# Performance work log

Hardware: AMD Instinct MI355X
Metric: run time of the kernel (lower is better)

Reference implementation:

```python
import jax, jax.numpy as jnp
import numpy as np

_EPS = 1e-5

def _ln(x, scale, shift):
    # Faithful to the module's custom layer norm: variance term is the SUM of
    # squared deviations over the feature dim (not the mean), and the affine is
    # scale * normed + shift with scale=b*, shift=s* (argument order as in source).
    m = jnp.mean(x, axis=-1, keepdims=True)
    d = x - m
    ssq = jnp.sum(d * d, axis=-1, keepdims=True)
    return scale * (d / jnp.sqrt(ssq + _EPS)) + shift


def setup_inputs() -> dict:
    key = jax.random.key(0)
    ks = jax.random.split(key, 12)
    B, T, I, H = 64, 512, 512, 512
    f32 = jnp.float32
    return {
        "x": jax.random.normal(ks[0], (B, T, I), f32),
        "hx": jax.random.normal(ks[1], (B, H), f32),
        "cx": jax.random.normal(ks[2], (B, H), f32),
        "Wi": jax.random.normal(ks[3], (4 * H, I), f32) / np.float32(np.sqrt(I)),
        "Wh": jax.random.normal(ks[4], (4 * H, H), f32) / np.float32(np.sqrt(H)),
        "bias": jax.random.normal(ks[5], (4 * H,), f32) * 0.1,
        "b1": jax.random.normal(ks[6], (4 * H,), f32) * 0.1,
        "b2": jax.random.normal(ks[7], (4 * H,), f32) * 0.1,
        "b3": jax.random.normal(ks[8], (H,), f32) * 0.1,
        "s1": 1.0 + jax.random.normal(ks[9], (4 * H,), f32) * 0.1,
        "s2": 1.0 + jax.random.normal(ks[10], (4 * H,), f32) * 0.1,
        "s3": 1.0 + jax.random.normal(ks[11], (H,), f32) * 0.1,
    }


def reference(x, hx, cx, Wi, Wh, bias, b1, b2, b3, s1, s2, s3):
    # x: [B, T, I] (batch_first). Work in time-major for the scan.
    xT = jnp.swapaxes(x, 0, 1)  # [T, B, I]
    # The input-projection layer norm has no cross-time dependency -> precompute.
    gi = _ln(jnp.einsum('tbi,gi->tbg', xT, Wi), b1, s1)  # [T, B, 4H]

    def step(carry, gi_t):
        h, c = carry
        gates = gi_t + _ln(h @ Wh.T, b2, s2) + bias  # [B, 4H]
        i, f, g, o = jnp.split(gates, 4, axis=-1)
        i = jax.nn.sigmoid(i)
        f = jax.nn.sigmoid(f)
        g = jnp.tanh(g)
        o = jax.nn.sigmoid(o)
        c_new = _ln(f * c + i * g, b3, s3)
        h_new = o * jnp.tanh(c_new)
        return (h_new, c_new), h_new

    (hy, cy), ys = jax.lax.scan(step, (hx, cx), gi)
    output = jnp.swapaxes(ys, 0, 1)  # back to [B, T, H]
    return output, hy, cy
```

## Files before the change

### kernel.cpp

```cpp
#include <hip/hip_runtime.h>
#include <cstdint>
#include <cstddef>


typedef float  f32x4 __attribute__((ext_vector_type(4)));
typedef __bf16 bf16x8 __attribute__((ext_vector_type(8)));
typedef unsigned int u32x4 __attribute__((ext_vector_type(4)));
typedef unsigned short u16x4 __attribute__((ext_vector_type(4)));

#define DEV __device__ __forceinline__

#define LD4_AGENT(dst, p) asm volatile("global_load_dwordx4 %0, %1, off sc1" : "=v"(dst) : "v"(p) : "memory")
#define ISSUE_U64(dst, p) asm volatile("global_load_dwordx2 %0, %1, off sc1" : "=v"(dst) : "v"(p) : "memory")
#define WAIT_VM(N) do{ asm volatile("s_waitcnt vmcnt(" #N ")" ::: "memory"); \
                       __builtin_amdgcn_sched_barrier(0);}while(0)
#define VM0_FENCE() do{ asm volatile("s_waitcnt vmcnt(0)" ::: "memory"); \
                        __builtin_amdgcn_sched_barrier(0); }while(0)

DEV unsigned short f2b(float f){
  unsigned int u = __builtin_bit_cast(unsigned int, f);
  unsigned int r = (u + 0x7FFFu + ((u >> 16) & 1u)) >> 16;
  return (unsigned short)r;
}
DEV float b2f(unsigned short s){
  unsigned int u = ((unsigned int)s) << 16;
  return __builtin_bit_cast(float, u);
}
DEV float tanh_fast(float x){
  const float e = __expf(2.f * x);
  return 1.f - 2.f * __builtin_amdgcn_rcpf(e + 1.f);
}
DEV float sigmoid_fast(float x){
  return __builtin_amdgcn_rcpf(1.f + __expf(-x));
}

__global__ __launch_bounds__(256) void conv_bf16(const float* __restrict__ src,
                                                 unsigned short* __restrict__ dst,
                                                 int n4){
  int i = blockIdx.x * 256 + threadIdx.x;
  if (i >= n4) return;
  f32x4 v = ((const f32x4*)src)[i];
  u16x4 o;
  #pragma unroll
  for (int j = 0; j < 4; ++j) o[j] = f2b(v[j]);
  ((u16x4*)dst)[i] = o;
}

__global__ __launch_bounds__(256, 2) void gemm_gi(const unsigned short* __restrict__ Xb,
                                                  const unsigned short* __restrict__ Wib,
                                                  unsigned short* __restrict__ Gp){
  __shared__ unsigned short As[128 * 48];
  __shared__ unsigned short Bs[128 * 48];
  const int tid = threadIdx.x;
  const int m0 = blockIdx.x * 128;
  const int n0 = blockIdx.y * 128;
  const int w = tid >> 6, lane = tid & 63;
  const int lr = lane & 15, lq = lane >> 4;
  const int wm = (w & 1) * 64, wn = (w >> 1) * 64;
  const int sr = tid >> 2;
  const int sc = (tid & 3) * 8;
  const unsigned short* gx = Xb + (size_t)(m0 + sr) * 512 + sc;
  const unsigned short* gw = Wib + (size_t)(n0 + sr) * 512 + sc;
  f32x4 acc[4][4] = {};
  for (int kb = 0; kb < 16; ++kb){
    u32x4 a0 = *(const u32x4*)(gx + kb * 32);
    u32x4 a1 = *(const u32x4*)(gx + 64 * 512 + kb * 32);
    u32x4 b0 = *(const u32x4*)(gw + kb * 32);
    u32x4 b1 = *(const u32x4*)(gw + 64 * 512 + kb * 32);
    __syncthreads();
    *(u32x4*)&As[sr * 48 + sc] = a0;
    *(u32x4*)&As[(sr + 64) * 48 + sc] = a1;
    *(u32x4*)&Bs[sr * 48 + sc] = b0;
    *(u32x4*)&Bs[(sr + 64) * 48 + sc] = b1;
    __syncthreads();
    bf16x8 af[4], bfv[4];
    #pragma unroll
    for (int mi = 0; mi < 4; ++mi) af[mi] = *(const bf16x8*)&As[(wm + mi * 16 + lr) * 48 + lq * 8];
    #pragma unroll
    for (int ni = 0; ni < 4; ++ni) bfv[ni] = *(const bf16x8*)&Bs[(wn + ni * 16 + lr) * 48 + lq * 8];
    #pragma unroll
    for (int mi = 0; mi < 4; ++mi)
      #pragma unroll
      for (int ni = 0; ni < 4; ++ni)
        acc[mi][ni] = __builtin_amdgcn_mfma_f32_16x16x32_bf16(af[mi], bfv[ni], acc[mi][ni], 0, 0, 0);
  }
  #pragma unroll
  for (int mi = 0; mi < 4; ++mi){
    const int rowb = m0 + wm + mi * 16 + lq * 4;
    #pragma unroll
    for (int ni = 0; ni < 4; ++ni){
      const int col = n0 + wn + ni * 16 + lr;
      #pragma unroll
      for (int r = 0; r < 4; ++r)
        Gp[(size_t)(rowb + r) * 2048 + col] = f2b(acc[mi][ni][r]);
    }
  }
}

__global__ __launch_bounds__(256) void ln_rows(unsigned short* __restrict__ G,
                                               const float* __restrict__ b1,
                                               const float* __restrict__ s1){
  const int row = blockIdx.x;
  const int tid = threadIdx.x;
  unsigned short* rp = G + (size_t)row * 2048 + tid * 8;
  u32x4 raw = *(const u32x4*)rp;
  float x[8];
  #pragma unroll
  for (int j = 0; j < 8; ++j){
    unsigned int word = raw[j >> 1];
    unsigned short us = (j & 1) ? (unsigned short)(word >> 16) : (unsigned short)(word & 0xFFFF);
    x[j] = b2f(us);
  }
  float s = 0.f, q = 0.f;
  #pragma unroll
  for (int j = 0; j < 8; ++j){ s += x[j]; q += x[j] * x[j]; }
  #pragma unroll
  for (int o = 1; o < 64; o <<= 1){ s += __shfl_xor(s, o); q += __shfl_xor(q, o); }
  __shared__ float ps[4][2];
  const int wv = tid >> 6;
  if ((tid & 63) == 0){ ps[wv][0] = s; ps[wv][1] = q; }
  __syncthreads();
  s = ps[0][0] + ps[1][0] + ps[2][0] + ps[3][0];
  q = ps[0][1] + ps[1][1] + ps[2][1] + ps[3][1];
  const float mu = s * (1.f / 2048.f);
  const float inv = rsqrtf((q - s * mu) + 1e-5f);
  const float* b1p = b1 + tid * 8;
  const float* s1p = s1 + tid * 8;
  u32x4 outw;
  #pragma unroll
  for (int j = 0; j < 4; ++j){
    float y0 = b1p[2 * j]     * ((x[2 * j]     - mu) * inv) + s1p[2 * j];
    float y1 = b1p[2 * j + 1] * ((x[2 * j + 1] - mu) * inv) + s1p[2 * j + 1];
    outw[j] = (unsigned int)f2b(y0) | ((unsigned int)f2b(y1) << 16);
  }
  *(u32x4*)rp = outw;
}

__global__ __launch_bounds__(512, 2) void lstm_rec(
    const unsigned short* __restrict__ Gi,
    const unsigned short* __restrict__ Whb,
    const float* __restrict__ bias,
    const float* __restrict__ b2, const float* __restrict__ s2,
    const float* __restrict__ b3, const float* __restrict__ s3,
    const float* __restrict__ hx,
    const float* __restrict__ cx,
    unsigned int* __restrict__ hbuf,
    unsigned long long* __restrict__ pF,
    unsigned long long* __restrict__ pA,
    unsigned long long* __restrict__ pCs,
    float* __restrict__ out){
  const int tid = threadIdx.x;
  const int tm = (blockIdx.x >> 1) & 3;
  const int ks = ((blockIdx.x >> 3) << 1) | (blockIdx.x & 1);
  const int w = tid >> 6;
  const int lane = tid & 63;
  const int lr = lane & 15, lq = lane >> 4;

  const int type = w >> 1;
  const int jloc = (w & 1) * 16 + lr;
  const int row_g = type * 512 + ks * 32 + jloc;
  const float b2r = b2[row_g];
  const float sbr = s2[row_g] + bias[row_g];

  bf16x8 bfr[16];
  {
    const unsigned short* wr = Whb + (size_t)row_g * 512 + lq * 8;
    #pragma unroll
    for (int kk = 0; kk < 16; ++kk) bfr[kk] = *(const bf16x8*)(wr + kk * 32);
  }

  const int cs = tid >> 5;
  const int cj = tid & 31;
  const int hcol = ks * 32 + cj;
  const int bidx = tm * 16 + cs;
  float c_val = cx[(size_t)bidx * 512 + hcol];
  const float b3j = b3[hcol], s3j = s3[hcol];

  const int psmp = 2 * w + (lane >> 5);
  const int pidx = lane & 31;
  const int pl_slice = (lane >> 1) & 15;
  const int pl_kind  = lane & 1;

  float b3c[16], s3c[16];
  #pragma unroll
  for (int q = 0; q < 4; ++q)
    #pragma unroll
    for (int j = 0; j < 4; ++j){
      const int c = 4 * pidx + 128 * q + j;
      b3c[4 * q + j] = b3[c];
      s3c[4 * q + j] = s3[c];
    }

  __shared__ unsigned short hlds[16 * 520];
  __shared__ float act[4][32][17];
  __shared__ float redA[8][16][2];
  __shared__ float stAl[16][2];

  float cc_own = 0.f, o_own = 0.f;

  for (int t = 0; t < 512; ++t){
    float giv[4];
    #pragma unroll
    for (int r = 0; r < 4; ++r){
      const int b = tm * 16 + lq * 4 + r;
      giv[r] = b2f(Gi[((size_t)b * 512 + t) * 2048 + row_g]);
    }

    if (t == 0){
      const float* hr = hx + (size_t)(tm * 16 + psmp) * 512;
      #pragma unroll
      for (int q = 0; q < 4; ++q){
        f32x4 hv4 = *(const f32x4*)(hr + 4 * pidx + 128 * q);
        unsigned long long pk = 0;
        #pragma unroll
        for (int j = 0; j < 4; ++j)
          pk |= (unsigned long long)f2b(hv4[j]) << (16 * j);
        *(unsigned long long*)&hlds[psmp * 520 + 4 * pidx + 128 * q] = pk;
      }
    } else {
      const unsigned int tg = (unsigned)t;
      const unsigned long long* fp = pF + (size_t)(t & 1) * 64 + tm * 16 + (lane & 15);
      const unsigned long long* sp =
          pCs + ((size_t)(t & 1) * 4 + tm) * 512 + pl_slice * 32 + psmp * 2 + pl_kind;
      unsigned long long fa, sa, fb, sb;
      unsigned long long sv;
      ISSUE_U64(fa, fp); ISSUE_U64(sa, sp);
      __builtin_amdgcn_s_sleep(12);
      ISSUE_U64(fb, fp); ISSUE_U64(sb, sp);
      for (;;){
        WAIT_VM(2);
        bool ok = ((unsigned)fa == tg) & ((unsigned)(sa >> 32) == tg);
        if (__all((int)ok)){ sv = sa; break; }
        ISSUE_U64(fa, fp); ISSUE_U64(sa, sp);
        WAIT_VM(2);
        ok = ((unsigned)fb == tg) & ((unsigned)(sb >> 32) == tg);
        if (__all((int)ok)){ sv = sb; break; }
        ISSUE_U64(fb, fp); ISSUE_U64(sb, sp);
      }
      const unsigned int* hsrc =
          hbuf + (size_t)(t & 1) * 32768 + (size_t)(tm * 16 + psmp) * 512;
      u32x4 pay[4];
      #pragma unroll
      for (int q = 0; q < 4; ++q) LD4_AGENT(pay[q], hsrc + 4 * pidx + 128 * q);
      float pv = __builtin_bit_cast(float, (unsigned)sv);
      #pragma unroll
      for (int o = 2; o < 32; o <<= 1) pv += __shfl_xor(pv, o);
      const float ov = __shfl_xor(pv, 1);
      const float S = pl_kind ? ov : pv;
      const float Q = pl_kind ? pv : ov;
      const float mu = S * (1.f / 512.f);
      const float inv = rsqrtf((Q - S * mu) + 1e-5f);
      c_val = b3j * ((cc_own - mu) * inv) + s3j;
      const float h_self = o_own * tanh_fast(c_val);
      out[((size_t)bidx * 512 + (t - 1)) * 512 + hcol] = h_self;
      VM0_FENCE();
      asm volatile("" :: "v"(fa), "v"(sa), "v"(fb), "v"(sb));
      #pragma unroll
      for (int q = 0; q < 4; ++q){
        unsigned long long pk = 0;
        #pragma unroll
        for (int j = 0; j < 4; ++j){
          const unsigned int v = pay[q][j];
          const float ccv = b2f((unsigned short)(v & 0xFFFF));
          const float oov = b2f((unsigned short)(v >> 16));
          const float h = oov * tanh_fast(b3c[4 * q + j] * ((ccv - mu) * inv) + s3c[4 * q + j]);
          pk |= (unsigned long long)f2b(h) << (16 * j);
        }
        *(unsigned long long*)&hlds[psmp * 520 + 4 * pidx + 128 * q] = pk;
      }
    }
    __syncthreads();

    f32x4 acc = {0.f, 0.f, 0.f, 0.f};
    #pragma unroll
    for (int kk = 0; kk < 16; ++kk){
      bf16x8 af = *(const bf16x8*)&hlds[lr * 520 + lq * 8 + kk * 32];
      acc = __builtin_amdgcn_mfma_f32_16x16x32_bf16(af, bfr[kk], acc, 0, 0, 0);
    }
    #pragma unroll
    for (int r = 0; r < 4; ++r){
      float s = acc[r], q = acc[r] * acc[r];
      #pragma unroll
      for (int o = 1; o < 16; o <<= 1){ s += __shfl_xor(s, o); q += __shfl_xor(q, o); }
      if (lr == 0){ redA[w][lq * 4 + r][0] = s; redA[w][lq * 4 + r][1] = q; }
    }
    __syncthreads();

    unsigned long long* slotA = pA + ((size_t)(t & 1) * 4 + tm) * 512;
    const unsigned int atag = (unsigned)(t + 1);
    if (w == 0 && lane < 32){
      const int smp = lane >> 1, kd = lane & 1;
      float Sp = 0.f;
      #pragma unroll
      for (int w2 = 0; w2 < 8; ++w2) Sp += redA[w2][smp][kd];
      const unsigned long long pvs = ((unsigned long long)atag << 32) |
          (unsigned long long)__builtin_bit_cast(unsigned int, Sp);
      __hip_atomic_store(slotA + (size_t)ks * 32 + lane, pvs,
                         __ATOMIC_RELAXED, __HIP_MEMORY_SCOPE_AGENT);
    }
    unsigned long long aa, ab;
    {
      const unsigned long long* ap = slotA + pl_slice * 32 + psmp * 2 + pl_kind;
      unsigned long long av;
      ISSUE_U64(aa, ap);
      __builtin_amdgcn_s_sleep(12);
      ISSUE_U64(ab, ap);
      for (;;){
        WAIT_VM(1);
        if (__all((int)((unsigned)(aa >> 32) == atag))){ av = aa; break; }
        ISSUE_U64(aa, ap);
        WAIT_VM(1);
        if (__all((int)((unsigned)(ab >> 32) == atag))){ av = ab; break; }
        ISSUE_U64(ab, ap);
      }
      float pv = __builtin_bit_cast(float, (unsigned)av);
      #pragma unroll
      for (int o = 2; o < 32; o <<= 1) pv += __shfl_xor(pv, o);
      const float ov = __shfl_xor(pv, 1);
      const float S = pl_kind ? ov : pv;
      const float Q = pl_kind ? pv : ov;
      if ((lane & 31) == 0){
        const float mu = S * (1.f / 2048.f);
        stAl[psmp][0] = mu;
        stAl[psmp][1] = rsqrtf((Q - S * mu) + 1e-5f);
      }
    }
    __syncthreads();

    #pragma unroll
    for (int r = 0; r < 4; ++r){
      const int s0 = lq * 4 + r;
      const float nv = (acc[r] - stAl[s0][0]) * stAl[s0][1];
      const float gv = giv[r] + b2r * nv + sbr;
      float a;
      if (type == 2) a = tanh_fast(gv);
      else           a = sigmoid_fast(gv);
      act[type][jloc][s0] = a;
    }
    __syncthreads();

    const float i_g = act[0][cj][cs];
    const float f_g = act[1][cj][cs];
    const float g_g = act[2][cj][cs];
    const float o_g = act[3][cj][cs];
    const float cc = f_g * c_val + i_g * g_g;
    const unsigned int ntag = (unsigned)(t + 1);
    const size_t np = (size_t)((t + 1) & 1);
    {
      const unsigned int pv32 = (unsigned int)f2b(cc) | ((unsigned int)f2b(o_g) << 16);
      __hip_atomic_store(hbuf + np * 32768 + (size_t)bidx * 512 + hcol, pv32,
                         __ATOMIC_RELAXED, __HIP_MEMORY_SCOPE_AGENT);
    }
    float sC = cc, qC = cc * cc;
    #pragma unroll
    for (int o = 1; o < 32; o <<= 1){ sC += __shfl_xor(sC, o); qC += __shfl_xor(qC, o); }
    unsigned long long* slotC = pCs + (np * 4 + tm) * 512;
    if ((lane & 31) < 2){
      const float v = (lane & 1) ? qC : sC;
      const unsigned long long pvs = ((unsigned long long)ntag << 32) |
          (unsigned long long)__builtin_bit_cast(unsigned int, v);
      __hip_atomic_store(slotC + (size_t)ks * 32 + cs * 2 + (lane & 1), pvs,
                         __ATOMIC_RELAXED, __HIP_MEMORY_SCOPE_AGENT);
    }
    VM0_FENCE();
    asm volatile("" :: "v"(aa), "v"(ab));
    __syncthreads();
    if (tid == 0)
      __hip_atomic_store(pF + np * 64 + tm * 16 + ks, (unsigned long long)ntag,
                         __ATOMIC_RELAXED, __HIP_MEMORY_SCOPE_AGENT);
    cc_own = cc; o_own = o_g;
  }

  {
    const unsigned long long* sp =
        pCs + ((size_t)0 * 4 + tm) * 512 + pl_slice * 32 + psmp * 2 + pl_kind;
    unsigned long long sv;
    for (;;){
      sv = __hip_atomic_load(sp, __ATOMIC_RELAXED, __HIP_MEMORY_SCOPE_AGENT);
      if (__all((int)((unsigned)(sv >> 32) == 512u))) break;
      __builtin_amdgcn_s_sleep(2);
    }
    float pv = __builtin_bit_cast(float, (unsigned)sv);
    #pragma unroll
    for (int o = 2; o < 32; o <<= 1) pv += __shfl_xor(pv, o);
    const float ov = __shfl_xor(pv, 1);
    const float S = pl_kind ? ov : pv;
    const float Q = pl_kind ? pv : ov;
    const float mu = S * (1.f / 512.f);
    const float inv = rsqrtf((Q - S * mu) + 1e-5f);
    const float cn = b3j * ((cc_own - mu) * inv) + s3j;
    const float h = o_own * tanh_fast(cn);
    out[((size_t)bidx * 512 + 511) * 512 + hcol] = h;
    out[16777216u + (size_t)bidx * 512 + hcol] = h;
    out[16777216u + 32768u + (size_t)bidx * 512 + hcol] = cn;
  }
}

extern "C" void kernel_launch(void* const* d_in, const int* in_sizes, int n_in,
                              void* d_out, int out_size, void* d_ws, size_t ws_size,
                              hipStream_t stream){
  (void)in_sizes; (void)n_in; (void)out_size; (void)ws_size;
  const float* x    = (const float*)d_in[0];
  const float* hx   = (const float*)d_in[1];
  const float* cx   = (const float*)d_in[2];
  const float* Wi   = (const float*)d_in[3];
  const float* Wh   = (const float*)d_in[4];
  const float* bias = (const float*)d_in[5];
  const float* b1   = (const float*)d_in[6];
  const float* b2   = (const float*)d_in[7];
  const float* b3   = (const float*)d_in[8];
  const float* s1   = (const float*)d_in[9];
  const float* s2   = (const float*)d_in[10];
  const float* s3   = (const float*)d_in[11];
  float* out = (float*)d_out;
  char* ws = (char*)d_ws;

  unsigned short*     xb   = (unsigned short*)(ws);
  unsigned short*     wib  = (unsigned short*)(ws + 33554432);
  unsigned short*     whb  = (unsigned short*)(ws + 35651584);
  unsigned short*     gp   = (unsigned short*)(ws + 37748736);
  unsigned int*       hbuf = (unsigned int*)(ws + 171966464);
  unsigned long long* pF   = (unsigned long long*)(ws + 172228608);
  unsigned long long* pA   = (unsigned long long*)(ws + 172490752);
  unsigned long long* pCs  = (unsigned long long*)(ws + 172523520);

  hipMemsetAsync(pF, 0, 327680, stream);
  conv_bf16<<<16384, 256, 0, stream>>>(x,  xb,  4194304);
  conv_bf16<<<1024,  256, 0, stream>>>(Wi, wib, 262144);
  conv_bf16<<<1024,  256, 0, stream>>>(Wh, whb, 262144);
  gemm_gi<<<dim3(256, 16, 1), 256, 0, stream>>>(xb, wib, gp);
  ln_rows<<<32768, 256, 0, stream>>>(gp, b1, s1);
  lstm_rec<<<64, 512, 0, stream>>>(gp, whb, bias, b2, s2, b3, s3, hx, cx,
                                   hbuf, pF, pA, pCs, out);
}
```

Baseline: 3.090 ms.

## Compute recurrent LayerNorm stats locally via Gram matrix, removing cross-block exchange

The sum and sum-of-squares of h@Wh^T across all 2048 gate outputs are rewritten algebraically. The sum becomes h·(column sums of Wh), and the squared sum becomes h^T (Wh^T Wh) h, using a 512x512 Gram matrix and column-sum vector precomputed by new transpose and gram GEMM kernels. Each block can then compute the LayerNorm statistics locally, which drops the per-timestep inter-block atomic publish and spin-wait on pA. In exchange each step does four extra MFMA tiles per wave reading the Gram matrix from global memory. Precision also changes, since the Gram matrix is stored in bf16 and the variance is computed as Q - S*mu.

```diff
diff --git a/kernel.cpp b/kernel.cpp
--- a/kernel.cpp
+++ b/kernel.cpp
@@ -136,9 +136,96 @@
   *(u32x4*)rp = outw;
 }
 
-__global__ __launch_bounds__(512, 2) void lstm_rec(
+__global__ __launch_bounds__(256) void transpose_wh(const unsigned short* __restrict__ src,
+                                                    unsigned short* __restrict__ dst,
+                                                    float* __restrict__ wbar){
+  __shared__ unsigned short t[64][65];
+  const int k0 = blockIdx.x * 64;
+  const int d0 = blockIdx.y * 64;
+  const int tr = threadIdx.x >> 2;
+  const int c  = threadIdx.x & 3;
+  const int tc = c * 16;
+  u32x4 a = *(const u32x4*)(src + (size_t)(k0 + tr) * 512 + d0 + tc);
+  u32x4 b = *(const u32x4*)(src + (size_t)(k0 + tr) * 512 + d0 + tc + 8);
+  #pragma unroll
+  for (int j = 0; j < 4; ++j){
+    t[tr][tc + 2 * j]         = (unsigned short)(a[j] & 0xFFFF);
+    t[tr][tc + 2 * j + 1]     = (unsigned short)(a[j] >> 16);
+    t[tr][tc + 8 + 2 * j]     = (unsigned short)(b[j] & 0xFFFF);
+    t[tr][tc + 8 + 2 * j + 1] = (unsigned short)(b[j] >> 16);
+  }
+  __syncthreads();
+  unsigned short tmp[16];
+  float s = 0.f;
+  #pragma unroll
+  for (int j = 0; j < 16; ++j){ tmp[j] = t[tc + j][tr]; s += b2f(tmp[j]); }
+  s += __shfl_xor(s, 1); s += __shfl_xor(s, 2);
+  if (c == 0) atomicAdd(&wbar[d0 + tr], s);
+  u32x4 o0, o1;
+  #pragma unroll
+  for (int j = 0; j < 4; ++j){
+    o0[j] = (unsigned)tmp[2 * j]     | ((unsigned)tmp[2 * j + 1] << 16);
+    o1[j] = (unsigned)tmp[8 + 2 * j] | ((unsigned)tmp[8 + 2 * j + 1] << 16);
+  }
+  *(u32x4*)(dst + (size_t)(d0 + tr) * 2048 + k0 + tc) = o0;
+  *(u32x4*)(dst + (size_t)(d0 + tr) * 2048 + k0 + tc + 8) = o1;
+}
+
+__global__ __launch_bounds__(256, 2) void gemm_gram(const unsigned short* __restrict__ WhT,
+                                                    unsigned short* __restrict__ Gb){
+  __shared__ unsigned short As[128 * 48];
+  __shared__ unsigned short Bs[128 * 48];
+  const int tid = threadIdx.x;
+  const int m0 = blockIdx.x * 128;
+  const int n0 = blockIdx.y * 128;
+  const int w = tid >> 6, lane = tid & 63;
+  const int lr = lane & 15, lq = lane >> 4;
+  const int wm = (w & 1) * 64, wn = (w >> 1) * 64;
+  const int sr = tid >> 2;
+  const int sc = (tid & 3) * 8;
+  const unsigned short* gx = WhT + (size_t)(m0 + sr) * 2048 + sc;
+  const unsigned short* gw = WhT + (size_t)(n0 + sr) * 2048 + sc;
+  f32x4 acc[4][4] = {};
+  for (int kb = 0; kb < 64; ++kb){
+    u32x4 a0 = *(const u32x4*)(gx + kb * 32);
+    u32x4 a1 = *(const u32x4*)(gx + 64 * 2048 + kb * 32);
+    u32x4 b0 = *(const u32x4*)(gw + kb * 32);
+    u32x4 b1 = *(const u32x4*)(gw + 64 * 2048 + kb * 32);
+    __syncthreads();
+    *(u32x4*)&As[sr * 48 + sc] = a0;
+    *(u32x4*)&As[(sr + 64) * 48 + sc] = a1;
+    *(u32x4*)&Bs[sr * 48 + sc] = b0;
+    *(u32x4*)&Bs[(sr + 64) * 48 + sc] = b1;
+    __syncthreads();
+    bf16x8 af[4], bfv[4];
+    #pragma unroll
+    for (int mi = 0; mi < 4; ++mi) af[mi] = *(const bf16x8*)&As[(wm + mi * 16 + lr) * 48 + lq * 8];
+    #pragma unroll
+    for (int ni = 0; ni < 4; ++ni) bfv[ni] = *(const bf16x8*)&Bs[(wn + ni * 16 + lr) * 48 + lq * 8];
+    #pragma unroll
+    for (int mi = 0; mi < 4; ++mi)
+      #pragma unroll
+      for (int ni = 0; ni < 4; ++ni)
+        acc[mi][ni] = __builtin_amdgcn_mfma_f32_16x16x32_bf16(af[mi], bfv[ni], acc[mi][ni], 0, 0, 0);
+  }
+  #pragma unroll
+  for (int mi = 0; mi < 4; ++mi){
+    const int rowb = m0 + wm + mi * 16 + lq * 4;
+    #pragma unroll
+    for (int ni = 0; ni < 4; ++ni){
+      const int col = n0 + wn + ni * 16 + lr;
+      #pragma unroll
+      for (int r = 0; r < 4; ++r)
+        Gb[(size_t)(rowb + r) * 512 + col] = f2b(acc[mi][ni][r]);
+    }
+  }
+}
+
+__global__ __launch_bounds__(512, 1) void lstm_rec(
     const unsigned short* __restrict__ Gi,
     const unsigned short* __restrict__ Whb,
+    const unsigned short* __restrict__ Gb,
+    const float* __restrict__ wbar,
     const float* __restrict__ bias,
     const float* __restrict__ b2, const float* __restrict__ s2,
     const float* __restrict__ b3, const float* __restrict__ s3,
@@ -146,7 +233,6 @@
     const float* __restrict__ cx,
     unsigned int* __restrict__ hbuf,
     unsigned long long* __restrict__ pF,
-    unsigned long long* __restrict__ pA,
     unsigned long long* __restrict__ pCs,
     float* __restrict__ out){
   const int tid = threadIdx.x;
@@ -168,6 +254,10 @@
     #pragma unroll
     for (int kk = 0; kk < 16; ++kk) bfr[kk] = *(const bf16x8*)(wr + kk * 32);
   }
+  const unsigned short* grow = Gb + (size_t)(w * 64 + lr) * 512 + lq * 8;
+  float wbarc[4];
+  #pragma unroll
+  for (int ni = 0; ni < 4; ++ni) wbarc[ni] = wbar[w * 64 + ni * 16 + lr];
 
   const int cs = tid >> 5;
   const int cj = tid & 31;
@@ -272,57 +362,45 @@
     __syncthreads();
 
     f32x4 acc = {0.f, 0.f, 0.f, 0.f};
+    f32x4 accv[4] = {};
     #pragma unroll
     for (int kk = 0; kk < 16; ++kk){
-      bf16x8 af = *(const bf16x8*)&hlds[lr * 520 + lq * 8 + kk * 32];
-      acc = __builtin_amdgcn_mfma_f32_16x16x32_bf16(af, bfr[kk], acc, 0, 0, 0);
+      bf16x8 hf = *(const bf16x8*)&hlds[lr * 520 + lq * 8 + kk * 32];
+      acc = __builtin_amdgcn_mfma_f32_16x16x32_bf16(hf, bfr[kk], acc, 0, 0, 0);
+      #pragma unroll
+      for (int ni = 0; ni < 4; ++ni){
+        bf16x8 gf = *(const bf16x8*)(grow + (size_t)ni * 16 * 512 + kk * 32);
+        accv[ni] = __builtin_amdgcn_mfma_f32_16x16x32_bf16(hf, gf, accv[ni], 0, 0, 0);
+      }
     }
     #pragma unroll
     for (int r = 0; r < 4; ++r){
-      float s = acc[r], q = acc[r] * acc[r];
-      #pragma unroll
-      for (int o = 1; o < 16; o <<= 1){ s += __shfl_xor(s, o); q += __shfl_xor(q, o); }
-      if (lr == 0){ redA[w][lq * 4 + r][0] = s; redA[w][lq * 4 + r][1] = q; }
-    }
-    __syncthreads();
-
-    unsigned long long* slotA = pA + ((size_t)(t & 1) * 4 + tm) * 512;
-    const unsigned int atag = (unsigned)(t + 1);
+      const int srow = lq * 4 + r;
+      float qp = 0.f, sp = 0.f;
+      #pragma unroll
+      for (int ni = 0; ni < 4; ++ni){
+        const float hval = b2f(hlds[srow * 520 + w * 64 + ni * 16 + lr]);
+        qp += accv[ni][r] * hval;
+        sp += wbarc[ni] * hval;
+      }
+      #pragma unroll
+      for (int o = 1; o < 16; o <<= 1){ qp += __shfl_xor(qp, o); sp += __shfl_xor(sp, o); }
+      if (lr == 0){ redA[w][srow][0] = sp; redA[w][srow][1] = qp; }
+    }
+    __syncthreads();
+
     if (w == 0 && lane < 32){
       const int smp = lane >> 1, kd = lane & 1;
-      float Sp = 0.f;
-      #pragma unroll
-      for (int w2 = 0; w2 < 8; ++w2) Sp += redA[w2][smp][kd];
-      const unsigned long long pvs = ((unsigned long long)atag << 32) |
-          (unsigned long long)__builtin_bit_cast(unsigned int, Sp);
-      __hip_atomic_store(slotA + (size_t)ks * 32 + lane, pvs,
-                         __ATOMIC_RELAXED, __HIP_MEMORY_SCOPE_AGENT);
-    }
-    unsigned long long aa, ab;
-    {
-      const unsigned long long* ap = slotA + pl_slice * 32 + psmp * 2 + pl_kind;
-      unsigned long long av;
-      ISSUE_U64(aa, ap);
-      __builtin_amdgcn_s_sleep(12);
-      ISSUE_U64(ab, ap);
-      for (;;){
-        WAIT_VM(1);
-        if (__all((int)((unsigned)(aa >> 32) == atag))){ av = aa; break; }
-        ISSUE_U64(aa, ap);
-        WAIT_VM(1);
-        if (__all((int)((unsigned)(ab >> 32) == atag))){ av = ab; break; }
-        ISSUE_U64(ab, ap);
-      }
-      float pv = __builtin_bit_cast(float, (unsigned)av);
-      #pragma unroll
-      for (int o = 2; o < 32; o <<= 1) pv += __shfl_xor(pv, o);
-      const float ov = __shfl_xor(pv, 1);
-      const float S = pl_kind ? ov : pv;
-      const float Q = pl_kind ? pv : ov;
-      if ((lane & 31) == 0){
+      float P = 0.f;
+      #pragma unroll
+      for (int w2 = 0; w2 < 8; ++w2) P += redA[w2][smp][kd];
+      const float ov = __shfl_xor(P, 1);
+      const float S = kd ? ov : P;
+      const float Q = kd ? P : ov;
+      if (kd == 0){
         const float mu = S * (1.f / 2048.f);
-        stAl[psmp][0] = mu;
-        stAl[psmp][1] = rsqrtf((Q - S * mu) + 1e-5f);
+        stAl[smp][0] = mu;
+        stAl[smp][1] = rsqrtf((Q - S * mu) + 1e-5f);
       }
     }
     __syncthreads();
@@ -363,7 +441,6 @@
                          __ATOMIC_RELAXED, __HIP_MEMORY_SCOPE_AGENT);
     }
     VM0_FENCE();
-    asm volatile("" :: "v"(aa), "v"(ab));
     __syncthreads();
     if (tid == 0)
       __hip_atomic_store(pF + np * 64 + tm * 16 + ks, (unsigned long long)ntag,
@@ -423,6 +500,10 @@
   unsigned long long* pF   = (unsigned long long*)(ws + 172228608);
   unsigned long long* pA   = (unsigned long long*)(ws + 172490752);
   unsigned long long* pCs  = (unsigned long long*)(ws + 172523520);
+  unsigned short*     whT  = (unsigned short*)(ws);
+  unsigned short*     Gb   = (unsigned short*)(ws + 2097152);
+  float*              wbar = (float*)(ws + 2621440);
+  (void)pA;
 
   hipMemsetAsync(pF, 0, 327680, stream);
   conv_bf16<<<16384, 256, 0, stream>>>(x,  xb,  4194304);
@@ -430,6 +511,9 @@
   conv_bf16<<<1024,  256, 0, stream>>>(Wh, whb, 262144);
   gemm_gi<<<dim3(256, 16, 1), 256, 0, stream>>>(xb, wib, gp);
   ln_rows<<<32768, 256, 0, stream>>>(gp, b1, s1);
-  lstm_rec<<<64, 512, 0, stream>>>(gp, whb, bias, b2, s2, b3, s3, hx, cx,
-                                   hbuf, pF, pA, pCs, out);
-}
+  hipMemsetAsync(wbar, 0, 2048, stream);
+  transpose_wh<<<dim3(32, 8, 1), 256, 0, stream>>>(whb, whT, wbar);
+  gemm_gram<<<dim3(4, 4, 1), 256, 0, stream>>>(whT, Gb);
+  lstm_rec<<<64, 512, 0, stream>>>(gp, whb, Gb, wbar, bias, b2, s2, b3, s3, hx, cx,
+                                   hbuf, pF, pCs, out);
+}
```

New measurement: 10.68 ms. 246% more time.
